# Kernel tuning notes

Measured on AMD Instinct MI355X. Metric: run time of the kernel, lower is better.

The kernel has to match this reference:

```python
import jax, jax.numpy as jnp
import numpy as np

ALPHA = 0.9
EPS = 1e-5
SEQ, BATCH, D_MODEL, FF_DIM = 2048, 16, 512, 2048


def _layer_norm(x, g, b):
    m = jnp.mean(x, axis=-1, keepdims=True)
    v = jnp.mean((x - m) ** 2, axis=-1, keepdims=True)
    return (x - m) * jax.lax.rsqrt(v + EPS) * g + b


def _decay_matrix(seq, dtype):
    # Closed form of the torch roll/flip/tril loop:
    #   W[i, j] = alpha^{i-j+1}            for j <= i
    #   W[i, i] += 1 - sum_{k=1}^{i+1} alpha^k   (diag correction)
    i = jnp.arange(seq)
    diff = i[:, None] - i[None, :]                       # [S, S]
    causal = diff >= 0
    expo = jnp.where(causal, diff + 1, 0).astype(dtype)
    W = jnp.where(causal, jnp.asarray(ALPHA, dtype) ** expo, 0.0)
    W = W + jnp.diag(1.0 - W.sum(axis=1))
    return W


def setup_inputs() -> dict:
    key = jax.random.key(0)
    ks = jax.random.split(key, 8)
    s = lambda fan: 1.0 / np.sqrt(fan)
    return {
        "x": jax.random.normal(ks[0], (SEQ, BATCH, D_MODEL), jnp.float32),
        "w_lin": jax.random.normal(ks[1], (D_MODEL, D_MODEL), jnp.float32) * s(D_MODEL),
        "b_lin": jax.random.normal(ks[2], (D_MODEL,), jnp.float32) * 0.01,
        "w1": jax.random.normal(ks[3], (FF_DIM, D_MODEL), jnp.float32) * s(D_MODEL),
        "b1": jax.random.normal(ks[4], (FF_DIM,), jnp.float32) * 0.01,
        "w2": jax.random.normal(ks[5], (D_MODEL, FF_DIM), jnp.float32) * s(FF_DIM),
        "b2": jax.random.normal(ks[6], (D_MODEL,), jnp.float32) * 0.01,
        "g1": jnp.ones((D_MODEL,), jnp.float32),
        "beta1": jnp.zeros((D_MODEL,), jnp.float32),
        "g2": jnp.ones((D_MODEL,), jnp.float32),
        "beta2": jnp.zeros((D_MODEL,), jnp.float32),
    }


def reference(x, w_lin, b_lin, w1, b1, w2, b2, g1, beta1, g2, beta2):
    seq = x.shape[0]
    W = _decay_matrix(seq, x.dtype)                      # [S, S]

    # attention sublayer (dropout = identity in eval)
    y = _layer_norm(x, g1, beta1)
    z = jnp.einsum("sbd,ed->sbe", y, w_lin) + b_lin       # projection
    attn = jnp.einsum("ih,hbd->ibd", W, z)                # causal exp-decay mixing
    x = x + attn

    # feed-forward sublayer
    y = _layer_norm(x, g2, beta2)
    h = jax.nn.relu(jnp.einsum("sbd,fd->sbf", y, w1) + b1)
    ff = jnp.einsum("sbf,df->sbd", h, w2) + b2
    return x + ff
```

## Files before the change

### kernel.cpp

```cpp
#include <hip/hip_runtime.h>

#define SEQ 2048
#define BATCH 16
#define DMODEL 512
#define FFDIM 2048
#define NTOK (SEQ * BATCH)
#define ALPHA 0.9f

typedef unsigned short u16;
typedef unsigned int u32;
typedef __attribute__((ext_vector_type(8))) short short8;
typedef __attribute__((ext_vector_type(4))) float f32x4;

__device__ __forceinline__ float bf2f(u16 u) {
    unsigned int v = ((unsigned int)u) << 16;
    return __builtin_bit_cast(float, v);
}
__device__ __forceinline__ u16 f2bf(float f) {
    unsigned int v = __builtin_bit_cast(unsigned int, f);
    v += 0x7fffu + ((v >> 16) & 1u);
    return (u16)(v >> 16);
}

__global__ __launch_bounds__(256) void cvt_kernel(const float* __restrict__ in,
                                                  u16* __restrict__ out, int n) {
    const int i = (blockIdx.x * 256 + threadIdx.x) * 4;
    if (i >= n) return;
    float4 v = *(const float4*)(in + i);
    ushort4 o;
    o.x = f2bf(v.x); o.y = f2bf(v.y); o.z = f2bf(v.z); o.w = f2bf(v.w);
    *(ushort4*)(out + i) = o;
}

__global__ __launch_bounds__(256) void ln_kernel(const float* __restrict__ xin,
                                                 const float* __restrict__ g,
                                                 const float* __restrict__ b,
                                                 u16* __restrict__ y) {
    const int lane = threadIdx.x & 63;
    const int wave = threadIdx.x >> 6;
    const long tok = (long)blockIdx.x * 4 + wave;
    const long off = tok * DMODEL + lane * 8;

    float f[8];
    {
        const float4* xp = (const float4*)(xin + off);
        float4 a = xp[0], c = xp[1];
        f[0] = a.x; f[1] = a.y; f[2] = a.z; f[3] = a.w;
        f[4] = c.x; f[5] = c.y; f[6] = c.z; f[7] = c.w;
    }
    float s = 0.f, s2 = 0.f;
#pragma unroll
    for (int i = 0; i < 8; i++) { s += f[i]; s2 += f[i] * f[i]; }
#pragma unroll
    for (int o = 32; o > 0; o >>= 1) {
        s += __shfl_xor(s, o, 64);
        s2 += __shfl_xor(s2, o, 64);
    }
    const float mean = s * (1.f / DMODEL);
    const float var = s2 * (1.f / DMODEL) - mean * mean;
    const float inv = rsqrtf(var + 1e-5f);

    const float4* gp = (const float4*)(g + lane * 8);
    const float4* bp = (const float4*)(b + lane * 8);
    float4 g0 = gp[0], g1 = gp[1], b0 = bp[0], b1 = bp[1];
    float gg[8] = {g0.x, g0.y, g0.z, g0.w, g1.x, g1.y, g1.z, g1.w};
    float bb[8] = {b0.x, b0.y, b0.z, b0.w, b1.x, b1.y, b1.z, b1.w};
    short8 ov;
#pragma unroll
    for (int i = 0; i < 8; i++)
        ov[i] = (short)f2bf((f[i] - mean) * inv * gg[i] + bb[i]);
    *(short8*)(y + off) = ov;
}

#define SCAN_L 64
#define SCAN_H 128
#define NCOLU (BATCH * DMODEL / 2)
__global__ __launch_bounds__(256) void scan_kernel(const u16* __restrict__ z,
                                                   const float* __restrict__ x,
                                                   float* __restrict__ x1) {
    const int colu = blockIdx.x * 256 + threadIdx.x;
    const int s0 = blockIdx.y * SCAN_L;

    const u32* zp = (const u32*)z;
    const float2* xp = (const float2*)x;
    float2* x1p = (float2*)x1;

    float r0 = 0.f, r1 = 0.f;

    {
        int sb = s0 - SCAN_H;
        if (sb < 0) sb = 0;
        const int nw = s0 - sb;
        if (nw > 0) {
            u32 zq[4];
#pragma unroll
            for (int j = 0; j < 4; j++) zq[j] = zp[(long)(sb + j) * NCOLU + colu];
            for (int i = 0; i < nw; i += 4) {
#pragma unroll
                for (int j = 0; j < 4; j++) {
                    const u32 zz = zq[j];
                    if (i + j + 4 < nw)
                        zq[j] = zp[(long)(sb + i + j + 4) * NCOLU + colu];
                    r0 = ALPHA * (bf2f((u16)(zz & 0xffffu)) + r0);
                    r1 = ALPHA * (bf2f((u16)(zz >> 16)) + r1);
                }
            }
        }
    }

    float ap = powf(ALPHA, (float)(s0 + 2));

    u32 zq[4];
    float2 xq[4];
#pragma unroll
    for (int j = 0; j < 4; j++) {
        zq[j] = zp[(long)(s0 + j) * NCOLU + colu];
        xq[j] = xp[(long)(s0 + j) * NCOLU + colu];
    }
#pragma unroll 4
    for (int i = 0; i < SCAN_L; i++) {
        const int sl = i & 3;
        const u32 zz = zq[sl];
        const float2 xx = xq[sl];
        if (i + 4 < SCAN_L) {
            zq[sl] = zp[(long)(s0 + i + 4) * NCOLU + colu];
            xq[sl] = xp[(long)(s0 + i + 4) * NCOLU + colu];
        }
        const float z0 = bf2f((u16)(zz & 0xffffu));
        const float z1 = bf2f((u16)(zz >> 16));
        r0 = ALPHA * (z0 + r0);
        r1 = ALPHA * (z1 + r1);
        const float c = 1.f - (ALPHA - ap) * 10.f;
        ap *= ALPHA;
        x1p[(long)(s0 + i) * NCOLU + colu] = (float2){xx.x + r0 + c * z0, xx.y + r1 + c * z1};
    }
}

#define BM 128
#define BN 128
#define BKK 32

typedef __attribute__((address_space(1))) unsigned int as1_u32;
typedef __attribute__((address_space(3))) unsigned int as3_u32;

__device__ __forceinline__ void gld_lds16(const void* g, const void* l) {
    __builtin_amdgcn_global_load_lds((as1_u32*)(unsigned long long)g,
                                     (as3_u32*)(unsigned int)(unsigned long long)l,
                                     16, 0, 0);
}

template <int EPI, bool OUT_F32>
__global__ __launch_bounds__(256, 3) void gemm128(const u16* __restrict__ A,
                                                  const u16* __restrict__ Bt,
                                                  const float* __restrict__ bias,
                                                  const float* __restrict__ resid,
                                                  void* __restrict__ C,
                                                  int M, int N, int K) {
    __shared__ alignas(16) u16 sA[3][BM * BKK];
    __shared__ alignas(16) u16 sB[3][BN * BKK];

    const int tid = threadIdx.x;
    const int lane = tid & 63;
    const int wave = tid >> 6;
    const int wr = wave >> 1;
    const int wc = wave & 1;
    const int l15 = lane & 15, q16 = lane >> 4;

    const int gy = gridDim.y;
    const int nwg = gridDim.x * gy;
    const int d = blockIdx.y * gridDim.x + blockIdx.x;
    const int wgid = (d & 7) * (nwg >> 3) + (d >> 3);
    const int m0 = (wgid / gy) * BM;
    const int n0 = (wgid % gy) * BN;

    const u16* gA[2];
    const u16* gB[2];
    int ldsoff[2];
#pragma unroll
    for (int i = 0; i < 2; i++) {
        const int ch = tid + i * 256;
        const int r = ch >> 2;
        const int oo = (ch & 3) ^ ((r >> 1) & 3);
        gA[i] = A + (long)(m0 + r) * K + oo * 8;
        gB[i] = Bt + (long)(n0 + r) * K + oo * 8;
        ldsoff[i] = ch * 8;
    }

    const int octk = (q16 ^ ((l15 >> 1) & 3)) * 8;
    const int rowA0 = wr * 64 + l15;
    const int rowB0 = wc * 64 + l15;

    f32x4 acc[4][4];
#pragma unroll
    for (int i = 0; i < 4; i++)
#pragma unroll
        for (int j = 0; j < 4; j++) acc[i][j] = (f32x4){0.f, 0.f, 0.f, 0.f};

    const int NT = K / BKK;

#pragma unroll
    for (int i = 0; i < 2; i++) gld_lds16(gA[i], &sA[0][ldsoff[i]]);
#pragma unroll
    for (int i = 0; i < 2; i++) gld_lds16(gB[i], &sB[0][ldsoff[i]]);
#pragma unroll
    for (int i = 0; i < 2; i++) gld_lds16(gA[i] + BKK, &sA[1][ldsoff[i]]);
#pragma unroll
    for (int i = 0; i < 2; i++) gld_lds16(gB[i] + BKK, &sB[1][ldsoff[i]]);

    int pb = 0;
#pragma unroll 1
    for (int t = 0; t < NT; ++t) {
        if (t + 2 < NT) {
            int ps = pb + 2; if (ps >= 3) ps -= 3;
            const int ko = (t + 2) * BKK;
#pragma unroll
            for (int i = 0; i < 2; i++) gld_lds16(gA[i] + ko, &sA[ps][ldsoff[i]]);
#pragma unroll
            for (int i = 0; i < 2; i++) gld_lds16(gB[i] + ko, &sB[ps][ldsoff[i]]);
            asm volatile("s_waitcnt vmcnt(8)" ::: "memory");
        } else if (t + 1 < NT) {
            asm volatile("s_waitcnt vmcnt(4)" ::: "memory");
        } else {
            asm volatile("s_waitcnt vmcnt(0)" ::: "memory");
        }
        __builtin_amdgcn_s_barrier();

        const u16* pa = &sA[pb][rowA0 * BKK + octk];
        const u16* pbb = &sB[pb][rowB0 * BKK + octk];

        short8 a[4], b[4];
#pragma unroll
        for (int i = 0; i < 4; i++) a[i] = *(const short8*)(pa + i * 16 * BKK);
#pragma unroll
        for (int j = 0; j < 4; j++) b[j] = *(const short8*)(pbb + j * 16 * BKK);
#pragma unroll
        for (int i = 0; i < 4; i++)
#pragma unroll
            for (int j = 0; j < 4; j++)
                acc[i][j] = __builtin_amdgcn_mfma_f32_16x16x32_bf16(a[i], b[j],
                                                                    acc[i][j], 0, 0, 0);
        __builtin_amdgcn_s_barrier();
        pb = (pb == 2) ? 0 : pb + 1;
    }

#pragma unroll
    for (int i = 0; i < 4; i++) {
        const int row0 = m0 + wr * 64 + i * 16 + q16 * 4;
#pragma unroll
        for (int j = 0; j < 4; j++) {
            const int col = n0 + wc * 64 + j * 16 + l15;
            const float bv = bias[col];
#pragma unroll
            for (int r = 0; r < 4; r++) {
                const long idx = (long)(row0 + r) * N + col;
                float v = acc[i][j][r] + bv;
                if (EPI == 1) v = fmaxf(v, 0.f);
                if (EPI == 2) v += resid[idx];
                if (OUT_F32)
                    ((float*)C)[idx] = v;
                else
                    ((u16*)C)[idx] = f2bf(v);
            }
        }
    }
}

extern "C" void kernel_launch(void* const* d_in, const int* in_sizes, int n_in,
                              void* d_out, int out_size, void* d_ws, size_t ws_size,
                              hipStream_t stream) {
    const float* x = (const float*)d_in[0];
    const float* w_lin = (const float*)d_in[1];
    const float* b_lin = (const float*)d_in[2];
    const float* w1 = (const float*)d_in[3];
    const float* b1 = (const float*)d_in[4];
    const float* w2 = (const float*)d_in[5];
    const float* b2 = (const float*)d_in[6];
    const float* g1 = (const float*)d_in[7];
    const float* be1 = (const float*)d_in[8];
    const float* g2 = (const float*)d_in[9];
    const float* be2 = (const float*)d_in[10];
    float* out = (float*)d_out;

    char* ws = (char*)d_ws;
    const size_t MB = 1024 * 1024;
    u16* y = (u16*)(ws);
    float* x1 = (float*)(ws + 32 * MB);
    u16* h = (u16*)(ws + 96 * MB);
    u16* z = h;
    u16* wb_lin = (u16*)(ws + 224 * MB);
    u16* wb1 = (u16*)(ws + 225 * MB);
    u16* wb2 = (u16*)(ws + 228 * MB);

    cvt_kernel<<<(DMODEL * DMODEL) / 1024, 256, 0, stream>>>(w_lin, wb_lin, DMODEL * DMODEL);
    cvt_kernel<<<(FFDIM * DMODEL) / 1024, 256, 0, stream>>>(w1, wb1, FFDIM * DMODEL);
    cvt_kernel<<<(DMODEL * FFDIM) / 1024, 256, 0, stream>>>(w2, wb2, DMODEL * FFDIM);

    ln_kernel<<<NTOK / 4, 256, 0, stream>>>(x, g1, be1, y);
    gemm128<0, false><<<dim3(NTOK / BM, DMODEL / BN), 256, 0, stream>>>(y, wb_lin, b_lin, nullptr,
                                                                       z, NTOK, DMODEL, DMODEL);
    scan_kernel<<<dim3(NCOLU / 256, SEQ / SCAN_L), 256, 0, stream>>>(z, x, x1);
    ln_kernel<<<NTOK / 4, 256, 0, stream>>>(x1, g2, be2, y);
    gemm128<1, false><<<dim3(NTOK / BM, FFDIM / BN), 256, 0, stream>>>(y, wb1, b1, nullptr, h,
                                                                      NTOK, FFDIM, DMODEL);
    gemm128<2, true><<<dim3(NTOK / BM, DMODEL / BN), 256, 0, stream>>>(h, wb2, b2, x1, out,
                                                                      NTOK, DMODEL, FFDIM);
}
```

Measured before the change: 444.1 us.

## Replace 128x128 GEMM with 256x256 eight-wave ping-pong pipelined kernel

Swaps the 128x128x32 triple-buffered GEMM for a 256x256x64 tile with 512 threads (8 waves, 2x4 layout). Each wave computes a 128x64 sub-tile, and the K step is split into four phases. Each phase interleaves global-to-LDS prefetch of the next stage with MFMA work under s_setprio and sched_barrier, using double buffering. The larger tile is meant to raise arithmetic intensity and cut global/LDS traffic per FLOP. In exchange it uses more registers (32 accumulators per wave) and launches fewer workgroups, e.g. 128x2 blocks for the N=512 GEMMs, which risks occupancy and tail effects.

```diff
diff --git a/kernel.cpp b/kernel.cpp
--- a/kernel.cpp
+++ b/kernel.cpp
@@ -136,9 +136,9 @@
     }
 }
 
-#define BM 128
-#define BN 128
-#define BKK 32
+#define BM 256
+#define BN 256
+#define BKK 64
 
 typedef __attribute__((address_space(1))) unsigned int as1_u32;
 typedef __attribute__((address_space(3))) unsigned int as3_u32;
@@ -150,20 +150,20 @@
 }
 
 template <int EPI, bool OUT_F32>
-__global__ __launch_bounds__(256, 3) void gemm128(const u16* __restrict__ A,
-                                                  const u16* __restrict__ Bt,
-                                                  const float* __restrict__ bias,
-                                                  const float* __restrict__ resid,
-                                                  void* __restrict__ C,
-                                                  int M, int N, int K) {
-    __shared__ alignas(16) u16 sA[3][BM * BKK];
-    __shared__ alignas(16) u16 sB[3][BN * BKK];
+__global__ __launch_bounds__(512, 2) void gemm8p(const u16* __restrict__ A,
+                                                 const u16* __restrict__ Bt,
+                                                 const float* __restrict__ bias,
+                                                 const float* __restrict__ resid,
+                                                 void* __restrict__ C,
+                                                 int M, int N, int K) {
+    __shared__ alignas(16) u16 sA[2][2][256 * 32];
+    __shared__ alignas(16) u16 sB[2][2][256 * 32];
 
     const int tid = threadIdx.x;
     const int lane = tid & 63;
     const int wave = tid >> 6;
-    const int wr = wave >> 1;
-    const int wc = wave & 1;
+    const int wr = wave >> 2;
+    const int wc = wave & 3;
     const int l15 = lane & 15, q16 = lane >> 4;
 
     const int gy = gridDim.y;
@@ -175,85 +175,115 @@
 
     const u16* gA[2];
     const u16* gB[2];
-    int ldsoff[2];
-#pragma unroll
-    for (int i = 0; i < 2; i++) {
-        const int ch = tid + i * 256;
-        const int r = ch >> 2;
-        const int oo = (ch & 3) ^ ((r >> 1) & 3);
-        gA[i] = A + (long)(m0 + r) * K + oo * 8;
-        gB[i] = Bt + (long)(n0 + r) * K + oo * 8;
-        ldsoff[i] = ch * 8;
-    }
-
-    const int octk = (q16 ^ ((l15 >> 1) & 3)) * 8;
-    const int rowA0 = wr * 64 + l15;
-    const int rowB0 = wc * 64 + l15;
-
-    f32x4 acc[4][4];
-#pragma unroll
-    for (int i = 0; i < 4; i++)
+    int dsto[2];
+#pragma unroll
+    for (int j = 0; j < 2; j++) {
+        const int o = tid + j * 512;
+        const int r = o >> 2;
+        const int c = (o & 3) ^ ((o >> 4) & 3);
+        gA[j] = A + (long)(m0 + r) * K + c * 8;
+        gB[j] = Bt + (long)(n0 + r) * K + c * 8;
+        dsto[j] = o * 8;
+    }
+
+    const int xoct = (q16 ^ ((l15 >> 2) & 3)) * 8;
+    const int rowA = wr * 128 + l15;
+    const int rowB = wc * 64 + l15;
+
+    f32x4 acc[8][4];
+#pragma unroll
+    for (int i = 0; i < 8; i++)
 #pragma unroll
         for (int j = 0; j < 4; j++) acc[i][j] = (f32x4){0.f, 0.f, 0.f, 0.f};
 
     const int NT = K / BKK;
 
-#pragma unroll
-    for (int i = 0; i < 2; i++) gld_lds16(gA[i], &sA[0][ldsoff[i]]);
-#pragma unroll
-    for (int i = 0; i < 2; i++) gld_lds16(gB[i], &sB[0][ldsoff[i]]);
-#pragma unroll
-    for (int i = 0; i < 2; i++) gld_lds16(gA[i] + BKK, &sA[1][ldsoff[i]]);
-#pragma unroll
-    for (int i = 0; i < 2; i++) gld_lds16(gB[i] + BKK, &sB[1][ldsoff[i]]);
-
-    int pb = 0;
+#define STG_A(bs, kh, koff)                                                 \
+    {                                                                       \
+        gld_lds16(gA[0] + (koff) + (kh) * 32, &sA[bs][kh][dsto[0]]);        \
+        gld_lds16(gA[1] + (koff) + (kh) * 32, &sA[bs][kh][dsto[1]]);        \
+    }
+#define STG_B(bs, kh, koff)                                                 \
+    {                                                                       \
+        gld_lds16(gB[0] + (koff) + (kh) * 32, &sB[bs][kh][dsto[0]]);        \
+        gld_lds16(gB[1] + (koff) + (kh) * 32, &sB[bs][kh][dsto[1]]);        \
+    }
+#define MFMA16(mh)                                                          \
+    {                                                                       \
+        __builtin_amdgcn_s_setprio(1);                                      \
+        _Pragma("unroll") for (int mi = 0; mi < 4; mi++)                    \
+            _Pragma("unroll") for (int nj = 0; nj < 4; nj++)                \
+                acc[(mh)*4 + mi][nj] = __builtin_amdgcn_mfma_f32_16x16x32_bf16( \
+                    af[mi], bf[nj], acc[(mh)*4 + mi][nj], 0, 0, 0);         \
+        __builtin_amdgcn_s_setprio(0);                                      \
+    }
+#define PHASE_END                                                           \
+    {                                                                       \
+        __builtin_amdgcn_sched_barrier(0);                                  \
+        __builtin_amdgcn_s_barrier();                                       \
+    }
+
+    STG_A(0, 0, 0); STG_B(0, 0, 0); STG_A(0, 1, 0); STG_B(0, 1, 0);
+    asm volatile("s_waitcnt vmcnt(4)" ::: "memory");
+    __builtin_amdgcn_s_barrier();
+
 #pragma unroll 1
     for (int t = 0; t < NT; ++t) {
-        if (t + 2 < NT) {
-            int ps = pb + 2; if (ps >= 3) ps -= 3;
-            const int ko = (t + 2) * BKK;
-#pragma unroll
-            for (int i = 0; i < 2; i++) gld_lds16(gA[i] + ko, &sA[ps][ldsoff[i]]);
-#pragma unroll
-            for (int i = 0; i < 2; i++) gld_lds16(gB[i] + ko, &sB[ps][ldsoff[i]]);
-            asm volatile("s_waitcnt vmcnt(8)" ::: "memory");
-        } else if (t + 1 < NT) {
-            asm volatile("s_waitcnt vmcnt(4)" ::: "memory");
-        } else {
-            asm volatile("s_waitcnt vmcnt(0)" ::: "memory");
-        }
-        __builtin_amdgcn_s_barrier();
-
-        const u16* pa = &sA[pb][rowA0 * BKK + octk];
-        const u16* pbb = &sB[pb][rowB0 * BKK + octk];
-
-        short8 a[4], b[4];
-#pragma unroll
-        for (int i = 0; i < 4; i++) a[i] = *(const short8*)(pa + i * 16 * BKK);
-#pragma unroll
-        for (int j = 0; j < 4; j++) b[j] = *(const short8*)(pbb + j * 16 * BKK);
-#pragma unroll
-        for (int i = 0; i < 4; i++)
-#pragma unroll
-            for (int j = 0; j < 4; j++)
-                acc[i][j] = __builtin_amdgcn_mfma_f32_16x16x32_bf16(a[i], b[j],
-                                                                    acc[i][j], 0, 0, 0);
-        __builtin_amdgcn_s_barrier();
-        pb = (pb == 2) ? 0 : pb + 1;
-    }
-
-#pragma unroll
-    for (int i = 0; i < 4; i++) {
-        const int row0 = m0 + wr * 64 + i * 16 + q16 * 4;
-#pragma unroll
-        for (int j = 0; j < 4; j++) {
-            const int col = n0 + wc * 64 + j * 16 + l15;
+        const int b = t & 1, bn = b ^ 1;
+        const int ko = (t + 1) * BKK;
+        const bool nx = (t + 1 < NT);
+        short8 af[4], bf[4];
+
+#pragma unroll
+        for (int nj = 0; nj < 4; nj++)
+            bf[nj] = *(const short8*)(&sB[b][0][(rowB + nj * 16) * 32 + xoct]);
+#pragma unroll
+        for (int mi = 0; mi < 4; mi++)
+            af[mi] = *(const short8*)(&sA[b][0][(rowA + mi * 16) * 32 + xoct]);
+        if (nx) STG_A(bn, 0, ko);
+        MFMA16(0);
+        PHASE_END;
+
+#pragma unroll
+        for (int mi = 0; mi < 4; mi++)
+            af[mi] = *(const short8*)(&sA[b][0][(rowA + 64 + mi * 16) * 32 + xoct]);
+        if (nx) STG_B(bn, 0, ko);
+        MFMA16(1);
+        if (nx) asm volatile("s_waitcnt vmcnt(4)" ::: "memory");
+        else    asm volatile("s_waitcnt vmcnt(0)" ::: "memory");
+        PHASE_END;
+
+#pragma unroll
+        for (int nj = 0; nj < 4; nj++)
+            bf[nj] = *(const short8*)(&sB[b][1][(rowB + nj * 16) * 32 + xoct]);
+#pragma unroll
+        for (int mi = 0; mi < 4; mi++)
+            af[mi] = *(const short8*)(&sA[b][1][(rowA + mi * 16) * 32 + xoct]);
+        if (nx) STG_A(bn, 1, ko);
+        MFMA16(0);
+        PHASE_END;
+
+#pragma unroll
+        for (int mi = 0; mi < 4; mi++)
+            af[mi] = *(const short8*)(&sA[b][1][(rowA + 64 + mi * 16) * 32 + xoct]);
+        if (nx) STG_B(bn, 1, ko);
+        MFMA16(1);
+        if (nx) asm volatile("s_waitcnt vmcnt(4)" ::: "memory");
+        else    asm volatile("s_waitcnt vmcnt(0)" ::: "memory");
+        PHASE_END;
+    }
+
+#pragma unroll
+    for (int mf = 0; mf < 8; mf++) {
+        const int row0 = m0 + wr * 128 + mf * 16 + q16 * 4;
+#pragma unroll
+        for (int nj = 0; nj < 4; nj++) {
+            const int col = n0 + wc * 64 + nj * 16 + l15;
             const float bv = bias[col];
 #pragma unroll
             for (int r = 0; r < 4; r++) {
                 const long idx = (long)(row0 + r) * N + col;
-                float v = acc[i][j][r] + bv;
+                float v = acc[mf][nj][r] + bv;
                 if (EPI == 1) v = fmaxf(v, 0.f);
                 if (EPI == 2) v += resid[idx];
                 if (OUT_F32)
@@ -263,6 +293,10 @@
             }
         }
     }
+#undef STG_A
+#undef STG_B
+#undef MFMA16
+#undef PHASE_END
 }
 
 extern "C" void kernel_launch(void* const* d_in, const int* in_sizes, int n_in,
@@ -296,12 +330,12 @@
     cvt_kernel<<<(DMODEL * FFDIM) / 1024, 256, 0, stream>>>(w2, wb2, DMODEL * FFDIM);
 
     ln_kernel<<<NTOK / 4, 256, 0, stream>>>(x, g1, be1, y);
-    gemm128<0, false><<<dim3(NTOK / BM, DMODEL / BN), 256, 0, stream>>>(y, wb_lin, b_lin, nullptr,
-                                                                       z, NTOK, DMODEL, DMODEL);
+    gemm8p<0, false><<<dim3(NTOK / BM, DMODEL / BN), 512, 0, stream>>>(y, wb_lin, b_lin, nullptr,
+                                                                      z, NTOK, DMODEL, DMODEL);
     scan_kernel<<<dim3(NCOLU / 256, SEQ / SCAN_L), 256, 0, stream>>>(z, x, x1);
     ln_kernel<<<NTOK / 4, 256, 0, stream>>>(x1, g2, be2, y);
-    gemm128<1, false><<<dim3(NTOK / BM, FFDIM / BN), 256, 0, stream>>>(y, wb1, b1, nullptr, h,
-                                                                      NTOK, FFDIM, DMODEL);
-    gemm128<2, true><<<dim3(NTOK / BM, DMODEL / BN), 256, 0, stream>>>(h, wb2, b2, x1, out,
-                                                                      NTOK, DMODEL, FFDIM);
-}
+    gemm8p<1, false><<<dim3(NTOK / BM, FFDIM / BN), 512, 0, stream>>>(y, wb1, b1, nullptr, h,
+                                                                     NTOK, FFDIM, DMODEL);
+    gemm8p<2, true><<<dim3(NTOK / BM, DMODEL / BN), 512, 0, stream>>>(h, wb2, b2, x1, out,
+                                                                     NTOK, DMODEL, FFDIM);
+}
```

After: 434.7 us. 2.1% less time.
